# Performance work log

Hardware: AMD Instinct MI355X
Metric: run time of the kernel (lower is better)

## Reference

```python
import jax, jax.numpy as jnp
import numpy as np

B, L, N, D, C = 256, 512, 64, 32, 100  # batch, latent_dim, num_concepts, box_dim, num_classes


def setup_inputs() -> dict:
    key = jax.random.key(0)
    ks = jax.random.split(key, 11)
    s = 0.02  # weight init scale
    return {
        "h": jax.random.normal(ks[0], (B, L), dtype=jnp.float32),
        "Wc": jax.random.normal(ks[1], (N, L, D), dtype=jnp.float32) * s,
        "bc": jax.random.normal(ks[2], (N, D), dtype=jnp.float32) * s,
        "Wo": jax.random.normal(ks[3], (N, L, D), dtype=jnp.float32) * s,
        "bo": jax.random.normal(ks[4], (N, D), dtype=jnp.float32) * s,
        "Wp": jax.random.normal(ks[5], (N, 2 * D), dtype=jnp.float32) * s,
        "bp": jax.random.normal(ks[6], (N,), dtype=jnp.float32) * s,
        "W1": jax.random.normal(ks[7], (N * 2 * D, C), dtype=jnp.float32) * s,
        "b1": jax.random.normal(ks[8], (C,), dtype=jnp.float32) * s,
        "W2": jax.random.normal(ks[9], (N * N, C), dtype=jnp.float32) * s,
        "b2": jax.random.normal(ks[10], (C,), dtype=jnp.float32) * s,
    }


def reference(h, Wc, bc, Wo, bo, Wp, bp, W1, b1, W2, b2):
    EPS = 1e-6
    batch = h.shape[0]
    # Batched per-concept projections (replaces N un-batched Linears)
    x_m = jnp.einsum('bl,nld->bnd', h, Wc) + bc                    # [B,N,D] centers
    delta = jax.nn.softplus(jnp.einsum('bl,nld->bnd', h, Wo) + bo)  # [B,N,D] offsets
    box = jnp.concatenate([x_m, delta], axis=-1)                    # [B,N,2D]
    # Per-concept probability heads
    p_hat = jax.nn.sigmoid(jnp.einsum('bnd,nd->bn', box, Wp) + bp)  # [B,N]
    # Pairwise intersection volumes, fully broadcast (replaces N^2 loop)
    lo = x_m - delta  # [B,N,D]
    hi = x_m + delta
    inter = jnp.minimum(hi[:, :, None, :], hi[:, None, :, :]) - \
            jnp.maximum(lo[:, :, None, :], lo[:, None, :, :])       # [B,N,N,D]
    inter_off = jax.nn.relu(inter) * 0.5
    vol_inter = jnp.prod(inter_off + EPS, axis=-1)                  # [B,N,N]
    vol = jnp.prod(delta + EPS, axis=-1)                            # [B,N]
    V = vol_inter / vol[:, None, :]                                 # V[b,i,j] = |i∩j|/|j|
    # Classification heads
    aligned_flat = (box * p_hat[..., None]).reshape(batch, -1)      # [B, N*2D]
    y_hat = aligned_flat @ W1 + b1 + V.reshape(batch, -1) @ W2 + b2  # [B,C]
    return y_hat, p_hat, V
```

## Files before the change

### kernel.cpp

```cpp
#include <hip/hip_runtime.h>
#include <hip/hip_bf16.h>
#include <cstdint>

constexpr int Bb = 256, Ll = 512, Nn = 64, Dd = 32, Cc = 100;
constexpr float EPS = 1e-6f;

typedef __attribute__((ext_vector_type(8))) short short8;
typedef __attribute__((ext_vector_type(4))) short short4v;
typedef __attribute__((ext_vector_type(4))) float f32x4;

__device__ __forceinline__ unsigned short f2bf(float f) {
  union { float f; uint32_t u; } v; v.f = f;
  uint32_t r = v.u + 0x7FFFu + ((v.u >> 16) & 1u);
  return (unsigned short)(r >> 16);
}

__global__ __launch_bounds__(256) void kA(
    const float* __restrict__ h,
    const float* __restrict__ Wc,
    const float* __restrict__ bc,
    const float* __restrict__ Wo,
    const float* __restrict__ bo,
    const float* __restrict__ Wp,
    const float* __restrict__ bp,
    const float* __restrict__ b1,
    const float* __restrict__ b2,
    float* __restrict__ xm_ws,
    float* __restrict__ dl_ws,
    unsigned short* __restrict__ abuf,
    float* __restrict__ out_ph,
    float* __restrict__ out_y)
{
  const int n  = blockIdx.x;
  const int bt = blockIdx.y * 64;
  const int t  = threadIdx.x;
  const int w  = t >> 6, l = t & 63;
  const int lr = l & 15, lg = l >> 4;

  {
    const int bid = blockIdx.x + Nn * blockIdx.y;
    if (t < Cc) out_y[bid * Cc + t] = b1[t] + b2[t];
  }

  __shared__ unsigned short hb[64][72];
  __shared__ unsigned short wbT[64][72];

  f32x4 acc[4] = {};

  const int hr = t >> 2,       hc  = (t & 3) * 16;
  const int wk = (t >> 3) * 2, wcq = (t & 7) * 4;
  const float* hsrc  = h  + (bt + hr) * Ll + hc;
  const float* wcsrc = Wc + n * (Ll * Dd) + wk * Dd + wcq;
  const float* wosrc = Wo + n * (Ll * Dd) + wk * Dd + wcq;

  float4 hp0, hp1, hp2, hp3, c0, c1, o0, o1;
  auto fetch = [&](int k0) {
    const float* hs = hsrc + k0;
    hp0 = *(const float4*)(hs);
    hp1 = *(const float4*)(hs + 4);
    hp2 = *(const float4*)(hs + 8);
    hp3 = *(const float4*)(hs + 12);
    const float* ws = wcsrc + k0 * Dd;
    c0 = *(const float4*)(ws);
    c1 = *(const float4*)(ws + Dd);
    const float* os = wosrc + k0 * Dd;
    o0 = *(const float4*)(os);
    o1 = *(const float4*)(os + Dd);
  };

  fetch(0);
  for (int ch = 0; ch < 8; ch++) {
    __syncthreads();
    {
      short8 s0, s1;
      s0[0] = (short)f2bf(hp0.x); s0[1] = (short)f2bf(hp0.y);
      s0[2] = (short)f2bf(hp0.z); s0[3] = (short)f2bf(hp0.w);
      s0[4] = (short)f2bf(hp1.x); s0[5] = (short)f2bf(hp1.y);
      s0[6] = (short)f2bf(hp1.z); s0[7] = (short)f2bf(hp1.w);
      s1[0] = (short)f2bf(hp2.x); s1[1] = (short)f2bf(hp2.y);
      s1[2] = (short)f2bf(hp2.z); s1[3] = (short)f2bf(hp2.w);
      s1[4] = (short)f2bf(hp3.x); s1[5] = (short)f2bf(hp3.y);
      s1[6] = (short)f2bf(hp3.z); s1[7] = (short)f2bf(hp3.w);
      *(short8*)&hb[hr][hc]     = s0;
      *(short8*)&hb[hr][hc + 8] = s1;
    }
    {
      const float* c0p = &c0.x; const float* c1p = &c1.x;
      const float* o0p = &o0.x; const float* o1p = &o1.x;
      #pragma unroll
      for (int i = 0; i < 4; i++) {
        unsigned int pc = (unsigned int)f2bf(c0p[i]) |
                          ((unsigned int)f2bf(c1p[i]) << 16);
        *(unsigned int*)&wbT[wcq + i][wk] = pc;
        unsigned int po = (unsigned int)f2bf(o0p[i]) |
                          ((unsigned int)f2bf(o1p[i]) << 16);
        *(unsigned int*)&wbT[32 + wcq + i][wk] = po;
      }
    }
    __syncthreads();
    if (ch < 7) fetch((ch + 1) * 64);
    const int arow = w * 16 + lr;
    #pragma unroll
    for (int ks = 0; ks < 2; ks++) {
      const int ko = ks * 32 + lg * 8;
      const short8 av = *(const short8*)&hb[arow][ko];
      #pragma unroll
      for (int nf = 0; nf < 4; nf++) {
        const short8 bv = *(const short8*)&wbT[nf * 16 + lr][ko];
        acc[nf] = __builtin_amdgcn_mfma_f32_16x16x32_bf16(av, bv, acc[nf],
                                                          0, 0, 0);
      }
    }
  }

  const float bc0 = bc[n * Dd + lr],      bc1 = bc[n * Dd + 16 + lr];
  const float bo0 = bo[n * Dd + lr],      bo1 = bo[n * Dd + 16 + lr];
  const float wp0 = Wp[n * 64 + lr],      wp1 = Wp[n * 64 + 16 + lr];
  const float wp2 = Wp[n * 64 + 32 + lr], wp3 = Wp[n * 64 + 48 + lr];
  const float bpv = bp[n];

  #pragma unroll
  for (int q = 0; q < 4; q++) {
    const int b = bt + w * 16 + lg * 4 + q;
    const float xm0  = acc[0][q] + bc0;
    const float xm1  = acc[1][q] + bc1;
    const float pre0 = acc[2][q] + bo0;
    const float pre1 = acc[3][q] + bo1;
    const float dl0 = fmaxf(pre0, 0.f) + log1pf(expf(-fabsf(pre0)));
    const float dl1 = fmaxf(pre1, 0.f) + log1pf(expf(-fabsf(pre1)));
    float* xp = xm_ws + b * 2048 + n * Dd;
    float* dp = dl_ws + b * 2048 + n * Dd;
    xp[lr] = xm0;  xp[16 + lr] = xm1;
    dp[lr] = dl0;  dp[16 + lr] = dl1;
    float pp = xm0 * wp0 + xm1 * wp1 + dl0 * wp2 + dl1 * wp3;
    pp += __shfl_xor(pp, 1);
    pp += __shfl_xor(pp, 2);
    pp += __shfl_xor(pp, 4);
    pp += __shfl_xor(pp, 8);
    const float ph = 1.f / (1.f + expf(-(pp + bpv)));
    unsigned short* ab = abuf + b * 8192 + n * 64;
    ab[lr]      = f2bf(xm0 * ph);
    ab[16 + lr] = f2bf(xm1 * ph);
    ab[32 + lr] = f2bf(dl0 * ph);
    ab[48 + lr] = f2bf(dl1 * ph);
    if (lr == 0) out_ph[b * 64 + n] = ph;
  }
}

__global__ __launch_bounds__(512) void kB(
    const float* __restrict__ xm_ws,
    const float* __restrict__ dl_ws,
    float* __restrict__ out_V,
    unsigned short* __restrict__ abuf)
{
  const int b = blockIdx.x, t = threadIdx.x;
  __shared__ float lo[64][36];
  __shared__ float hi[64][36];

  {
    const int n = t >> 3, dd = (t & 7) * 4;
    float4 x = *(const float4*)(xm_ws + b * 2048 + n * Dd + dd);
    float4 g = *(const float4*)(dl_ws + b * 2048 + n * Dd + dd);
    lo[n][dd + 0] = x.x - g.x;  hi[n][dd + 0] = x.x + g.x;
    lo[n][dd + 1] = x.y - g.y;  hi[n][dd + 1] = x.y + g.y;
    lo[n][dd + 2] = x.z - g.z;  hi[n][dd + 2] = x.z + g.z;
    lo[n][dd + 3] = x.w - g.w;  hi[n][dd + 3] = x.w + g.w;
  }
  __syncthreads();

  const int j  = t & 63;
  const int wv = t >> 6;

  float4 lj[8], hj[8];
  #pragma unroll
  for (int q = 0; q < 8; q++) {
    lj[q] = *(const float4*)&lo[j][q * 4];
    hj[q] = *(const float4*)&hi[j][q * 4];
  }
  float pr = 1.f;
  #pragma unroll
  for (int q = 0; q < 8; q++) {
    pr *= ((hj[q].x - lj[q].x) * 0.5f + EPS);
    pr *= ((hj[q].y - lj[q].y) * 0.5f + EPS);
    pr *= ((hj[q].z - lj[q].z) * 0.5f + EPS);
    pr *= ((hj[q].w - lj[q].w) * 0.5f + EPS);
  }
  const float rv = 1.f / pr;

  #pragma unroll 1
  for (int it = 0; it < 8; it++) {
    const int i = wv * 8 + it;
    float prod = 1.f;
    #pragma unroll
    for (int q = 0; q < 8; q++) {
      const float4 hv = *(const float4*)&hi[i][q * 4];
      const float4 lv = *(const float4*)&lo[i][q * 4];
      float v0 = fmaxf((fminf(hv.x, hj[q].x) - fmaxf(lv.x, lj[q].x)) * 0.5f + EPS, EPS);
      float v1 = fmaxf((fminf(hv.y, hj[q].y) - fmaxf(lv.y, lj[q].y)) * 0.5f + EPS, EPS);
      float v2 = fmaxf((fminf(hv.z, hj[q].z) - fmaxf(lv.z, lj[q].z)) * 0.5f + EPS, EPS);
      float v3 = fmaxf((fminf(hv.w, hj[q].w) - fmaxf(lv.w, lj[q].w)) * 0.5f + EPS, EPS);
      prod *= v0 * v1 * v2 * v3;
    }
    const float V = prod * rv;
    out_V[b * 4096 + i * 64 + j] = V;
    abuf[b * 8192 + 4096 + i * 64 + j] = f2bf(V);
  }
}

__global__ __launch_bounds__(256) void kC(
    const unsigned short* __restrict__ abuf,
    const float* __restrict__ W1,
    const float* __restrict__ W2,
    float* __restrict__ out_y)
{
  const int Mg = blockIdx.x;
  const int s  = blockIdx.y;
  const bool isV = (s >= 32);
  const int m0 = (s & 31) * 128;
  const float* __restrict__ W = isV ? W2 : W1;
  const int b0 = Mg * 64;

  __shared__ unsigned short Ab[64][76];
  __shared__ unsigned short Wb[112][76];

  const int t = threadIdx.x;
  const int w = t >> 6, l = t & 63;
  const int lr = l & 15, lg = l >> 4;

  f32x4 acc[7] = {};

  const int ar = t >> 2, ak = (t & 3) * 16;
  const unsigned short* asrc =
      abuf + (b0 + ar) * 8192 + (isV ? 4096 : 0) + m0 + ak;
  const int wc = t & 127, half = t >> 7;

  short8 a0, a1;
  float wv[32];

  auto fetch = [&](int ch) {
    const int kb = ch * 64;
    a0 = *(const short8*)(asrc + kb);
    a1 = *(const short8*)(asrc + kb + 8);
    if (wc < Cc) {
      const float* wp = W + (m0 + kb + half * 32) * Cc + wc;
      #pragma unroll
      for (int i = 0; i < 32; i++) wv[i] = wp[i * Cc];
    }
  };

  fetch(0);
  #pragma unroll
  for (int ch = 0; ch < 2; ch++) {
    __syncthreads();
    *(short8*)&Ab[ar][ak]     = a0;
    *(short8*)&Ab[ar][ak + 8] = a1;
    if (wc < 112) {
      #pragma unroll
      for (int q8 = 0; q8 < 8; q8++) {
        short4v pk;
        if (wc < Cc) {
          pk[0] = (short)f2bf(wv[q8 * 4 + 0]);
          pk[1] = (short)f2bf(wv[q8 * 4 + 1]);
          pk[2] = (short)f2bf(wv[q8 * 4 + 2]);
          pk[3] = (short)f2bf(wv[q8 * 4 + 3]);
        } else {
          pk[0] = 0; pk[1] = 0; pk[2] = 0; pk[3] = 0;
        }
        *(short4v*)&Wb[wc][half * 32 + q8 * 4] = pk;
      }
    }
    __syncthreads();
    if (ch == 0) fetch(1);
    #pragma unroll
    for (int ks = 0; ks < 2; ks++) {
      const int ko = ks * 32 + lg * 8;
      const short8 av = *(const short8*)&Ab[w * 16 + lr][ko];
      #pragma unroll
      for (int nf = 0; nf < 7; nf++) {
        const short8 bv = *(const short8*)&Wb[nf * 16 + lr][ko];
        acc[nf] = __builtin_amdgcn_mfma_f32_16x16x32_bf16(av, bv, acc[nf],
                                                          0, 0, 0);
      }
    }
  }

  #pragma unroll
  for (int nf = 0; nf < 7; nf++) {
    const int col = nf * 16 + lr;
    if (col < Cc) {
      #pragma unroll
      for (int q = 0; q < 4; q++) {
        const int row = b0 + w * 16 + lg * 4 + q;
        atomicAdd(out_y + row * Cc + col, acc[nf][q]);
      }
    }
  }
}

extern "C" void kernel_launch(void* const* d_in, const int* in_sizes, int n_in,
                              void* d_out, int out_size, void* d_ws, size_t ws_size,
                              hipStream_t stream) {
  const float* h  = (const float*)d_in[0];
  const float* Wc = (const float*)d_in[1];
  const float* bc = (const float*)d_in[2];
  const float* Wo = (const float*)d_in[3];
  const float* bo = (const float*)d_in[4];
  const float* Wp = (const float*)d_in[5];
  const float* bp = (const float*)d_in[6];
  const float* W1 = (const float*)d_in[7];
  const float* b1 = (const float*)d_in[8];
  const float* W2 = (const float*)d_in[9];
  const float* b2 = (const float*)d_in[10];

  float* out    = (float*)d_out;
  float* out_y  = out;
  float* out_ph = out + Bb * Cc;
  float* out_V  = out + Bb * Cc + Bb * Nn;

  float* xm = (float*)d_ws;
  float* dl = xm + Bb * Nn * Dd;
  unsigned short* abuf = (unsigned short*)(dl + Bb * Nn * Dd);

  kA<<<dim3(Nn, Bb / 64), 256, 0, stream>>>(h, Wc, bc, Wo, bo, Wp, bp,
                                            b1, b2, xm, dl, abuf, out_ph, out_y);
  kB<<<Bb, 512, 0, stream>>>(xm, dl, out_V, abuf);
  kC<<<dim3(4, 64), 256, 0, stream>>>(abuf, W1, W2, out_y);
}
```

Before: 48.30 us.

## Split K across two thread groups in projection and classifier GEMM kernels

```diff
diff --git a/kernel.cpp b/kernel.cpp
--- a/kernel.cpp
+++ b/kernel.cpp
@@ -15,7 +15,7 @@
   return (unsigned short)(r >> 16);
 }
 
-__global__ __launch_bounds__(256) void kA(
+__global__ __launch_bounds__(512) void kA(
     const float* __restrict__ h,
     const float* __restrict__ Wc,
     const float* __restrict__ bc,
@@ -34,7 +34,9 @@
   const int n  = blockIdx.x;
   const int bt = blockIdx.y * 64;
   const int t  = threadIdx.x;
-  const int w  = t >> 6, l = t & 63;
+  const int kg = t >> 8;
+  const int tl = t & 255;
+  const int w  = tl >> 6, l = tl & 63;
   const int lr = l & 15, lg = l >> 4;
 
   {
@@ -42,13 +44,18 @@
     if (t < Cc) out_y[bid * Cc + t] = b1[t] + b2[t];
   }
 
-  __shared__ unsigned short hb[64][72];
-  __shared__ unsigned short wbT[64][72];
+  __shared__ union USmA {
+    struct {
+      unsigned short hb[2][64][72];
+      unsigned short wbT[2][64][72];
+    } s;
+    float red[16][264];
+  } u;
 
   f32x4 acc[4] = {};
 
-  const int hr = t >> 2,       hc  = (t & 3) * 16;
-  const int wk = (t >> 3) * 2, wcq = (t & 7) * 4;
+  const int hr = tl >> 2,       hc  = (tl & 3) * 16;
+  const int wk = (tl >> 3) * 2, wcq = (tl & 7) * 4;
   const float* hsrc  = h  + (bt + hr) * Ll + hc;
   const float* wcsrc = Wc + n * (Ll * Dd) + wk * Dd + wcq;
   const float* wosrc = Wo + n * (Ll * Dd) + wk * Dd + wcq;
@@ -68,8 +75,8 @@
     o1 = *(const float4*)(os + Dd);
   };
 
-  fetch(0);
-  for (int ch = 0; ch < 8; ch++) {
+  fetch(kg * 256);
+  for (int ch = 0; ch < 4; ch++) {
     __syncthreads();
     {
       short8 s0, s1;
@@ -81,8 +88,8 @@
       s1[2] = (short)f2bf(hp2.z); s1[3] = (short)f2bf(hp2.w);
       s1[4] = (short)f2bf(hp3.x); s1[5] = (short)f2bf(hp3.y);
       s1[6] = (short)f2bf(hp3.z); s1[7] = (short)f2bf(hp3.w);
-      *(short8*)&hb[hr][hc]     = s0;
-      *(short8*)&hb[hr][hc + 8] = s1;
+      *(short8*)&u.s.hb[kg][hr][hc]     = s0;
+      *(short8*)&u.s.hb[kg][hr][hc + 8] = s1;
     }
     {
       const float* c0p = &c0.x; const float* c1p = &c1.x;
@@ -91,59 +98,69 @@
       for (int i = 0; i < 4; i++) {
         unsigned int pc = (unsigned int)f2bf(c0p[i]) |
                           ((unsigned int)f2bf(c1p[i]) << 16);
-        *(unsigned int*)&wbT[wcq + i][wk] = pc;
+        *(unsigned int*)&u.s.wbT[kg][wcq + i][wk] = pc;
         unsigned int po = (unsigned int)f2bf(o0p[i]) |
                           ((unsigned int)f2bf(o1p[i]) << 16);
-        *(unsigned int*)&wbT[32 + wcq + i][wk] = po;
+        *(unsigned int*)&u.s.wbT[kg][32 + wcq + i][wk] = po;
       }
     }
     __syncthreads();
-    if (ch < 7) fetch((ch + 1) * 64);
+    if (ch < 3) fetch(kg * 256 + (ch + 1) * 64);
     const int arow = w * 16 + lr;
     #pragma unroll
     for (int ks = 0; ks < 2; ks++) {
       const int ko = ks * 32 + lg * 8;
-      const short8 av = *(const short8*)&hb[arow][ko];
+      const short8 av = *(const short8*)&u.s.hb[kg][arow][ko];
       #pragma unroll
       for (int nf = 0; nf < 4; nf++) {
-        const short8 bv = *(const short8*)&wbT[nf * 16 + lr][ko];
+        const short8 bv = *(const short8*)&u.s.wbT[kg][nf * 16 + lr][ko];
         acc[nf] = __builtin_amdgcn_mfma_f32_16x16x32_bf16(av, bv, acc[nf],
                                                           0, 0, 0);
       }
     }
   }
 
-  const float bc0 = bc[n * Dd + lr],      bc1 = bc[n * Dd + 16 + lr];
-  const float bo0 = bo[n * Dd + lr],      bo1 = bo[n * Dd + 16 + lr];
-  const float wp0 = Wp[n * 64 + lr],      wp1 = Wp[n * 64 + 16 + lr];
-  const float wp2 = Wp[n * 64 + 32 + lr], wp3 = Wp[n * 64 + 48 + lr];
-  const float bpv = bp[n];
-
-  #pragma unroll
-  for (int q = 0; q < 4; q++) {
-    const int b = bt + w * 16 + lg * 4 + q;
-    const float xm0  = acc[0][q] + bc0;
-    const float xm1  = acc[1][q] + bc1;
-    const float pre0 = acc[2][q] + bo0;
-    const float pre1 = acc[3][q] + bo1;
-    const float dl0 = fmaxf(pre0, 0.f) + log1pf(expf(-fabsf(pre0)));
-    const float dl1 = fmaxf(pre1, 0.f) + log1pf(expf(-fabsf(pre1)));
-    float* xp = xm_ws + b * 2048 + n * Dd;
-    float* dp = dl_ws + b * 2048 + n * Dd;
-    xp[lr] = xm0;  xp[16 + lr] = xm1;
-    dp[lr] = dl0;  dp[16 + lr] = dl1;
-    float pp = xm0 * wp0 + xm1 * wp1 + dl0 * wp2 + dl1 * wp3;
-    pp += __shfl_xor(pp, 1);
-    pp += __shfl_xor(pp, 2);
-    pp += __shfl_xor(pp, 4);
-    pp += __shfl_xor(pp, 8);
-    const float ph = 1.f / (1.f + expf(-(pp + bpv)));
-    unsigned short* ab = abuf + b * 8192 + n * 64;
-    ab[lr]      = f2bf(xm0 * ph);
-    ab[16 + lr] = f2bf(xm1 * ph);
-    ab[32 + lr] = f2bf(dl0 * ph);
-    ab[48 + lr] = f2bf(dl1 * ph);
-    if (lr == 0) out_ph[b * 64 + n] = ph;
+  __syncthreads();
+  if (kg == 1) {
+    #pragma unroll
+    for (int nf = 0; nf < 4; nf++)
+      #pragma unroll
+      for (int q = 0; q < 4; q++) u.red[nf * 4 + q][tl] = acc[nf][q];
+  }
+  __syncthreads();
+  if (kg == 0) {
+    const float bc0 = bc[n * Dd + lr],      bc1 = bc[n * Dd + 16 + lr];
+    const float bo0 = bo[n * Dd + lr],      bo1 = bo[n * Dd + 16 + lr];
+    const float wp0 = Wp[n * 64 + lr],      wp1 = Wp[n * 64 + 16 + lr];
+    const float wp2 = Wp[n * 64 + 32 + lr], wp3 = Wp[n * 64 + 48 + lr];
+    const float bpv = bp[n];
+
+    #pragma unroll
+    for (int q = 0; q < 4; q++) {
+      const int b = bt + w * 16 + lg * 4 + q;
+      const float xm0  = acc[0][q] + u.red[q][tl]      + bc0;
+      const float xm1  = acc[1][q] + u.red[4 + q][tl]  + bc1;
+      const float pre0 = acc[2][q] + u.red[8 + q][tl]  + bo0;
+      const float pre1 = acc[3][q] + u.red[12 + q][tl] + bo1;
+      const float dl0 = fmaxf(pre0, 0.f) + log1pf(expf(-fabsf(pre0)));
+      const float dl1 = fmaxf(pre1, 0.f) + log1pf(expf(-fabsf(pre1)));
+      float* xp = xm_ws + b * 2048 + n * Dd;
+      float* dp = dl_ws + b * 2048 + n * Dd;
+      xp[lr] = xm0;  xp[16 + lr] = xm1;
+      dp[lr] = dl0;  dp[16 + lr] = dl1;
+      float pp = xm0 * wp0 + xm1 * wp1 + dl0 * wp2 + dl1 * wp3;
+      pp += __shfl_xor(pp, 1);
+      pp += __shfl_xor(pp, 2);
+      pp += __shfl_xor(pp, 4);
+      pp += __shfl_xor(pp, 8);
+      const float ph = 1.f / (1.f + expf(-(pp + bpv)));
+      unsigned short* ab = abuf + b * 8192 + n * 64;
+      ab[lr]      = f2bf(xm0 * ph);
+      ab[16 + lr] = f2bf(xm1 * ph);
+      ab[32 + lr] = f2bf(dl0 * ph);
+      ab[48 + lr] = f2bf(dl1 * ph);
+      if (lr == 0) out_ph[b * 64 + n] = ph;
+    }
   }
 }
 
@@ -207,7 +224,7 @@
   }
 }
 
-__global__ __launch_bounds__(256) void kC(
+__global__ __launch_bounds__(512) void kC(
     const unsigned short* __restrict__ abuf,
     const float* __restrict__ W1,
     const float* __restrict__ W2,
@@ -220,78 +237,85 @@
   const float* __restrict__ W = isV ? W2 : W1;
   const int b0 = Mg * 64;
 
-  __shared__ unsigned short Ab[64][76];
-  __shared__ unsigned short Wb[112][76];
-
-  const int t = threadIdx.x;
-  const int w = t >> 6, l = t & 63;
+  const int t  = threadIdx.x;
+  const int kg = t >> 8;
+  const int tl = t & 255;
+  const int w  = tl >> 6, l = tl & 63;
   const int lr = l & 15, lg = l >> 4;
 
+  __shared__ union USmC {
+    struct {
+      unsigned short Ab[2][64][76];
+      unsigned short Wb[2][112][76];
+    } s;
+    float red[28][264];
+  } u;
+
   f32x4 acc[7] = {};
 
-  const int ar = t >> 2, ak = (t & 3) * 16;
+  const int ar = tl >> 2, ak = (tl & 3) * 16;
   const unsigned short* asrc =
-      abuf + (b0 + ar) * 8192 + (isV ? 4096 : 0) + m0 + ak;
-  const int wc = t & 127, half = t >> 7;
-
-  short8 a0, a1;
+      abuf + (b0 + ar) * 8192 + (isV ? 4096 : 0) + m0 + kg * 64 + ak;
+  const int wc = tl & 127, half = tl >> 7;
+
+  const short8 a0 = *(const short8*)(asrc);
+  const short8 a1 = *(const short8*)(asrc + 8);
   float wv[32];
-
-  auto fetch = [&](int ch) {
-    const int kb = ch * 64;
-    a0 = *(const short8*)(asrc + kb);
-    a1 = *(const short8*)(asrc + kb + 8);
-    if (wc < Cc) {
-      const float* wp = W + (m0 + kb + half * 32) * Cc + wc;
+  if (wc < Cc) {
+    const float* wp = W + (m0 + kg * 64 + half * 32) * Cc + wc;
+    #pragma unroll
+    for (int i = 0; i < 32; i++) wv[i] = wp[i * Cc];
+  }
+
+  *(short8*)&u.s.Ab[kg][ar][ak]     = a0;
+  *(short8*)&u.s.Ab[kg][ar][ak + 8] = a1;
+  if (wc < 112) {
+    #pragma unroll
+    for (int q8 = 0; q8 < 8; q8++) {
+      short4v pk;
+      if (wc < Cc) {
+        pk[0] = (short)f2bf(wv[q8 * 4 + 0]);
+        pk[1] = (short)f2bf(wv[q8 * 4 + 1]);
+        pk[2] = (short)f2bf(wv[q8 * 4 + 2]);
+        pk[3] = (short)f2bf(wv[q8 * 4 + 3]);
+      } else {
+        pk[0] = 0; pk[1] = 0; pk[2] = 0; pk[3] = 0;
+      }
+      *(short4v*)&u.s.Wb[kg][wc][half * 32 + q8 * 4] = pk;
+    }
+  }
+  __syncthreads();
+
+  #pragma unroll
+  for (int ks = 0; ks < 2; ks++) {
+    const int ko = ks * 32 + lg * 8;
+    const short8 av = *(const short8*)&u.s.Ab[kg][w * 16 + lr][ko];
+    #pragma unroll
+    for (int nf = 0; nf < 7; nf++) {
+      const short8 bv = *(const short8*)&u.s.Wb[kg][nf * 16 + lr][ko];
+      acc[nf] = __builtin_amdgcn_mfma_f32_16x16x32_bf16(av, bv, acc[nf],
+                                                        0, 0, 0);
+    }
+  }
+
+  __syncthreads();
+  if (kg == 1) {
+    #pragma unroll
+    for (int nf = 0; nf < 7; nf++)
       #pragma unroll
-      for (int i = 0; i < 32; i++) wv[i] = wp[i * Cc];
-    }
-  };
-
-  fetch(0);
-  #pragma unroll
-  for (int ch = 0; ch < 2; ch++) {
-    __syncthreads();
-    *(short8*)&Ab[ar][ak]     = a0;
-    *(short8*)&Ab[ar][ak + 8] = a1;
-    if (wc < 112) {
-      #pragma unroll
-      for (int q8 = 0; q8 < 8; q8++) {
-        short4v pk;
-        if (wc < Cc) {
-          pk[0] = (short)f2bf(wv[q8 * 4 + 0]);
-          pk[1] = (short)f2bf(wv[q8 * 4 + 1]);
-          pk[2] = (short)f2bf(wv[q8 * 4 + 2]);
-          pk[3] = (short)f2bf(wv[q8 * 4 + 3]);
-        } else {
-          pk[0] = 0; pk[1] = 0; pk[2] = 0; pk[3] = 0;
+      for (int q = 0; q < 4; q++) u.red[nf * 4 + q][tl] = acc[nf][q];
+  }
+  __syncthreads();
+  if (kg == 0) {
+    #pragma unroll
+    for (int nf = 0; nf < 7; nf++) {
+      const int col = nf * 16 + lr;
+      if (col < Cc) {
+        #pragma unroll
+        for (int q = 0; q < 4; q++) {
+          const int row = b0 + w * 16 + lg * 4 + q;
+          atomicAdd(out_y + row * Cc + col, acc[nf][q] + u.red[nf * 4 + q][tl]);
         }
-        *(short4v*)&Wb[wc][half * 32 + q8 * 4] = pk;
-      }
-    }
-    __syncthreads();
-    if (ch == 0) fetch(1);
-    #pragma unroll
-    for (int ks = 0; ks < 2; ks++) {
-      const int ko = ks * 32 + lg * 8;
-      const short8 av = *(const short8*)&Ab[w * 16 + lr][ko];
-      #pragma unroll
-      for (int nf = 0; nf < 7; nf++) {
-        const short8 bv = *(const short8*)&Wb[nf * 16 + lr][ko];
-        acc[nf] = __builtin_amdgcn_mfma_f32_16x16x32_bf16(av, bv, acc[nf],
-                                                          0, 0, 0);
-      }
-    }
-  }
-
-  #pragma unroll
-  for (int nf = 0; nf < 7; nf++) {
-    const int col = nf * 16 + lr;
-    if (col < Cc) {
-      #pragma unroll
-      for (int q = 0; q < 4; q++) {
-        const int row = b0 + w * 16 + lg * 4 + q;
-        atomicAdd(out_y + row * Cc + col, acc[nf][q]);
       }
     }
   }
@@ -321,8 +345,8 @@
   float* dl = xm + Bb * Nn * Dd;
   unsigned short* abuf = (unsigned short*)(dl + Bb * Nn * Dd);
 
-  kA<<<dim3(Nn, Bb / 64), 256, 0, stream>>>(h, Wc, bc, Wo, bo, Wp, bp,
+  kA<<<dim3(Nn, Bb / 64), 512, 0, stream>>>(h, Wc, bc, Wo, bo, Wp, bp,
                                             b1, b2, xm, dl, abuf, out_ph, out_y);
   kB<<<Bb, 512, 0, stream>>>(xm, dl, out_V, abuf);
-  kC<<<dim3(4, 64), 256, 0, stream>>>(abuf, W1, W2, out_y);
-}
+  kC<<<dim3(4, 64), 512, 0, stream>>>(abuf, W1, W2, out_y);
+}
```

Result: no change. 48.54 us (+0.5%).
